# Performance work log

Hardware: AMD Instinct MI355X
Metric: run time of the kernel (lower is better)

The kernel has to match this reference:

```python
import jax, jax.numpy as jnp
import numpy as np
import math

NUM_HEADS = 16
ROPE_BASE = 10000.0


def apply_rope(t):
    # t: [B, H, S, D] with D even. Interleaved-pair rotary embedding (torchtune-style).
    D = t.shape[-1]
    S = t.shape[-2]
    inv_freq = 1.0 / (ROPE_BASE ** (jnp.arange(0, D, 2, dtype=jnp.float32) / D))  # [D/2]
    angles = jnp.arange(S, dtype=jnp.float32)[:, None] * inv_freq[None, :]  # [S, D/2]
    cos = jnp.cos(angles).astype(t.dtype)  # [S, D/2]
    sin = jnp.sin(angles).astype(t.dtype)
    t1 = t[..., 0::2]  # [B, H, S, D/2]
    t2 = t[..., 1::2]
    r1 = t1 * cos - t2 * sin
    r2 = t1 * sin + t2 * cos
    # interleave back
    out = jnp.stack([r1, r2], axis=-1).reshape(t.shape)
    return out


def setup_inputs() -> dict:
    key = jax.random.key(0)
    ks = jax.random.split(key, 6)
    B, S, D = 4, 2048, 2048
    s_in = 1.0 / math.sqrt(D)
    x = jax.random.normal(ks[0], (B, S, D), dtype=jnp.float32)
    wq = jax.random.normal(ks[1], (D, D), dtype=jnp.float32) * s_in
    wk = jax.random.normal(ks[2], (D, D), dtype=jnp.float32) * s_in
    wv = jax.random.normal(ks[3], (D, D), dtype=jnp.float32) * s_in
    wo = jax.random.normal(ks[4], (D, D), dtype=jnp.float32) * s_in
    bo = jnp.zeros((D,), dtype=jnp.float32)
    return {"x": x, "wq": wq, "wk": wk, "wv": wv, "wo": wo, "bo": bo}


def reference(x, wq, wk, wv, wo, bo):
    B, S, D = x.shape
    H = NUM_HEADS
    hd = D // H
    # QKV projections (nn.Linear: y = x @ W^T)
    q = (x @ wq.T).reshape(B, S, H, hd).transpose(0, 2, 1, 3)  # [B,H,S,hd]
    k = (x @ wk.T).reshape(B, S, H, hd).transpose(0, 2, 1, 3)
    v = (x @ wv.T).reshape(B, S, H, hd).transpose(0, 2, 1, 3)
    q = apply_rope(q)
    k = apply_rope(k)
    # causal SDPA (dropout_p = 0 in eval)
    scale = 1.0 / math.sqrt(hd)
    scores = jnp.einsum('bhqd,bhkd->bhqk', q, k) * scale  # [B,H,S,S]
    causal = jnp.tril(jnp.ones((S, S), dtype=bool))
    scores = jnp.where(causal, scores, jnp.finfo(scores.dtype).min)
    attn = jax.nn.softmax(scores, axis=-1)
    ctx = jnp.einsum('bhqk,bhkd->bqhd', attn, v).reshape(B, S, D)
    return ctx @ wo.T + bo
```

## Files before the change

kernel.cpp:

```cpp
#include <hip/hip_runtime.h>

typedef short short8 __attribute__((ext_vector_type(8)));
typedef float f32x4 __attribute__((ext_vector_type(4)));
typedef unsigned int u32x4 __attribute__((ext_vector_type(4)));
typedef unsigned short u16x4 __attribute__((ext_vector_type(4)));
typedef unsigned short u16x8 __attribute__((ext_vector_type(8)));

__device__ __forceinline__ unsigned short f2bf(float f) {
  unsigned int u = __builtin_bit_cast(unsigned int, f);
  u += 0x7fffu + ((u >> 16) & 1u);
  return (unsigned short)(u >> 16);
}
__device__ __forceinline__ float bf2f(unsigned short h) {
  unsigned int u = ((unsigned int)h) << 16;
  return __builtin_bit_cast(float, u);
}

__device__ __forceinline__ void gl16(const unsigned short* g, unsigned short* l) {
  __builtin_amdgcn_global_load_lds((const __attribute__((address_space(1))) unsigned int*)g,
                                   (__attribute__((address_space(3))) unsigned int*)l, 16, 0, 0);
}

#define BB 4
#define SS 2048
#define DD 2048
#define HH 16
#define HD 128
#define MM (BB * SS)

__global__ void cast_all(const float* __restrict__ x, const float* __restrict__ wq,
                         const float* __restrict__ wk, const float* __restrict__ wv,
                         const float* __restrict__ wo, unsigned short* __restrict__ xb,
                         unsigned short* __restrict__ wqb, unsigned short* __restrict__ wkb,
                         unsigned short* __restrict__ wvb, unsigned short* __restrict__ wob) {
  int i = blockIdx.x * blockDim.x + threadIdx.x;
  const int X4 = (MM * DD) / 4;
  const int W4 = (DD * DD) / 4;
  const float* src;
  unsigned short* dst;
  int off;
  if (i < X4) {
    src = x; dst = xb; off = i;
  } else {
    int t = i - X4;
    int w = t >> 20;
    off = t & (W4 - 1);
    src = (w == 0) ? wq : (w == 1) ? wk : (w == 2) ? wv : wo;
    dst = (w == 0) ? wqb : (w == 1) ? wkb : (w == 2) ? wvb : wob;
  }
  f32x4 v = ((const f32x4*)src)[off];
  u16x4 o;
  o[0] = f2bf(v[0]); o[1] = f2bf(v[1]); o[2] = f2bf(v[2]); o[3] = f2bf(v[3]);
  ((u16x4*)dst)[off] = o;
}

#define STGH(P, R0, t, h, moff)                                                     \
  do {                                                                              \
    const unsigned short* _s =                                                      \
        (P) + (size_t)((R0) + (h) * 128 + srow) * DD + (size_t)((t) * 64 + scol);   \
    gl16(_s, lds + (moff) + (h) * 8192 + wvi * 512);                                \
    gl16(_s + (size_t)64 * DD, lds + (moff) + (h) * 8192 + 4096 + wvi * 512);       \
  } while (0)

#define BARRIER asm volatile("s_barrier" ::: "memory")

__device__ __forceinline__ void gemm_core(const unsigned short* __restrict__ Ap,
                                          const unsigned short* __restrict__ Bp,
                                          unsigned short* lds, int rt, int ct,
                                          f32x4 (&acc)[8][4]) {
  const int tid = threadIdx.x;
  const int lane = tid & 63, wvi = tid >> 6;
  const int wm = wvi >> 2, wn = wvi & 3;
  const int quad = lane >> 4, l16 = lane & 15;
  const int srow = wvi * 8 + (lane >> 3);
  const int scol = ((lane & 7) ^ (lane >> 3)) << 3;
  const int ck0 = (quad ^ (l16 & 7)) << 3;
  const int ck1 = ((4 + quad) ^ (l16 & 7)) << 3;
  const int aro = (wm * 128 + l16) << 6;
  const int bro = (wn * 64 + l16) << 6;
  const int rb = rt * 256, cb = ct * 256;

#pragma unroll
  for (int i = 0; i < 8; ++i)
#pragma unroll
    for (int j = 0; j < 4; ++j) acc[i][j] = f32x4{0.f, 0.f, 0.f, 0.f};

  STGH(Bp, cb, 0, 0, 16384);
  STGH(Bp, cb, 0, 1, 16384);
  STGH(Ap, rb, 0, 0, 0);
  STGH(Ap, rb, 0, 1, 0);
  STGH(Bp, cb, 1, 0, 49152);
  STGH(Bp, cb, 1, 1, 49152);
  asm volatile("s_waitcnt vmcnt(4)" ::: "memory");
  BARRIER;

#pragma unroll 2
  for (int t = 0; t < 32; ++t) {
    const unsigned short* ab = lds + ((t & 1) << 15);
    const unsigned short* bb = ab + 16384;
    const int pn = ((t + 1) & 1) << 15;
    const int pc = ((t & 1) << 15) + 16384;
    short8 aq[4][2], b0f[2][2], b1f[2][2];

#pragma unroll
    for (int mi = 0; mi < 4; ++mi) {
      aq[mi][0] = __builtin_bit_cast(short8, *(const u32x4*)(ab + aro + mi * 1024 + ck0));
      aq[mi][1] = __builtin_bit_cast(short8, *(const u32x4*)(ab + aro + mi * 1024 + ck1));
    }
#pragma unroll
    for (int ni = 0; ni < 2; ++ni) {
      b0f[ni][0] = __builtin_bit_cast(short8, *(const u32x4*)(bb + bro + ni * 1024 + ck0));
      b0f[ni][1] = __builtin_bit_cast(short8, *(const u32x4*)(bb + bro + ni * 1024 + ck1));
    }
    if (t < 31) STGH(Ap, rb, t + 1, 0, pn);
    BARRIER;
    __builtin_amdgcn_s_setprio(1);
#pragma unroll
    for (int k = 0; k < 2; ++k)
#pragma unroll
      for (int mi = 0; mi < 4; ++mi)
#pragma unroll
        for (int ni = 0; ni < 2; ++ni)
          acc[mi][ni] =
              __builtin_amdgcn_mfma_f32_16x16x32_bf16(aq[mi][k], b0f[ni][k], acc[mi][ni], 0, 0, 0);
    __builtin_amdgcn_s_setprio(0);
    BARRIER;

#pragma unroll
    for (int ni = 0; ni < 2; ++ni) {
      b1f[ni][0] = __builtin_bit_cast(short8, *(const u32x4*)(bb + bro + 2048 + ni * 1024 + ck0));
      b1f[ni][1] = __builtin_bit_cast(short8, *(const u32x4*)(bb + bro + 2048 + ni * 1024 + ck1));
    }
    if (t < 31) STGH(Ap, rb, t + 1, 1, pn);
    BARRIER;
    __builtin_amdgcn_s_setprio(1);
#pragma unroll
    for (int k = 0; k < 2; ++k)
#pragma unroll
      for (int mi = 0; mi < 4; ++mi)
#pragma unroll
        for (int ni = 0; ni < 2; ++ni)
          acc[mi][2 + ni] = __builtin_amdgcn_mfma_f32_16x16x32_bf16(aq[mi][k], b1f[ni][k],
                                                                    acc[mi][2 + ni], 0, 0, 0);
    __builtin_amdgcn_s_setprio(0);
    BARRIER;

#pragma unroll
    for (int mi = 0; mi < 4; ++mi) {
      aq[mi][0] = __builtin_bit_cast(short8, *(const u32x4*)(ab + aro + 4096 + mi * 1024 + ck0));
      aq[mi][1] = __builtin_bit_cast(short8, *(const u32x4*)(ab + aro + 4096 + mi * 1024 + ck1));
    }
    if (t < 30) STGH(Bp, cb, t + 2, 0, pc);
    BARRIER;
    __builtin_amdgcn_s_setprio(1);
#pragma unroll
    for (int k = 0; k < 2; ++k)
#pragma unroll
      for (int mi = 0; mi < 4; ++mi)
#pragma unroll
        for (int ni = 0; ni < 2; ++ni)
          acc[4 + mi][2 + ni] = __builtin_amdgcn_mfma_f32_16x16x32_bf16(
              aq[mi][k], b1f[ni][k], acc[4 + mi][2 + ni], 0, 0, 0);
    __builtin_amdgcn_s_setprio(0);
    BARRIER;

    if (t < 30) STGH(Bp, cb, t + 2, 1, pc);
    BARRIER;
    __builtin_amdgcn_s_setprio(1);
#pragma unroll
    for (int k = 0; k < 2; ++k)
#pragma unroll
      for (int mi = 0; mi < 4; ++mi)
#pragma unroll
        for (int ni = 0; ni < 2; ++ni)
          acc[4 + mi][ni] = __builtin_amdgcn_mfma_f32_16x16x32_bf16(aq[mi][k], b0f[ni][k],
                                                                    acc[4 + mi][ni], 0, 0, 0);
    __builtin_amdgcn_s_setprio(0);
    if (t < 30) {
      asm volatile("s_waitcnt vmcnt(4)" ::: "memory");
      BARRIER;
    } else if (t == 30) {
      asm volatile("s_waitcnt vmcnt(0)" ::: "memory");
      BARRIER;
    }
  }
}

__global__ __launch_bounds__(512, 2) void gemm_qkv(const unsigned short* __restrict__ A,
                                                   const unsigned short* __restrict__ W0,
                                                   const unsigned short* __restrict__ W1,
                                                   const unsigned short* __restrict__ W2,
                                                   unsigned short* __restrict__ q_out,
                                                   unsigned short* __restrict__ k_out,
                                                   unsigned short* __restrict__ v_out) {
  __shared__ unsigned short lds[65536];
  const int id = (blockIdx.z << 8) | (blockIdx.y << 3) | blockIdx.x;
  const int nid = (id & 7) * 96 + (id >> 3);
  const int z = nid >> 8;
  const int rt = (nid & 255) >> 3, ct = nid & 7;
  const unsigned short* W = (z == 0) ? W0 : (z == 1) ? W1 : W2;
  unsigned short* outb = (z == 0) ? q_out : (z == 1) ? k_out : v_out;
  f32x4 acc[8][4];
  gemm_core(A, W, lds, rt, ct, acc);

  const int tid = threadIdx.x;
  const int lane = tid & 63, wvi = tid >> 6;
  const int wm = wvi >> 2, wn = wvi & 3;
  const int quad = lane >> 4, l16 = lane & 15;

  if (z == 2) {
#pragma unroll
    for (int mi = 0; mi < 8; ++mi)
#pragma unroll
      for (int ni = 0; ni < 4; ++ni)
#pragma unroll
        for (int r = 0; r < 4; ++r) {
          int row_g = rt * 256 + wm * 128 + mi * 16 + quad * 4 + r;
          int col_g = ct * 256 + wn * 64 + ni * 16 + l16;
          int b = row_g >> 11, s = row_g & (SS - 1);
          int h = col_g >> 7, d = col_g & (HD - 1);
          outb[(((size_t)(b * HH + h)) * SS + (size_t)s) * HD + (size_t)d] = f2bf(acc[mi][ni][r]);
        }
  } else {
    const float psc = (z == 0) ? 0.08838834764831845f : 1.0f;
    const bool odd = (l16 & 1) != 0;
    const float nl = -0.14391156831212936f;
    float inv4[4];
#pragma unroll
    for (int ni = 0; ni < 4; ++ni)
      inv4[ni] = __expf((float)((((wn * 64 + ni * 16 + l16) & 127) >> 1)) * nl);
#pragma unroll
    for (int mi = 0; mi < 8; ++mi)
#pragma unroll
      for (int ni = 0; ni < 4; ++ni)
#pragma unroll
        for (int r = 0; r < 4; ++r) {
          int row_g = rt * 256 + wm * 128 + mi * 16 + quad * 4 + r;
          int col_g = ct * 256 + wn * 64 + ni * 16 + l16;
          int b = row_g >> 11, s = row_g & (SS - 1);
          int h = col_g >> 7, d = col_g & (HD - 1);
          float v = acc[mi][ni][r];
          float p = __shfl_xor(v, 1, 64);
          float ang = (float)s * inv4[ni];
          float cs = __cosf(ang), sn = __sinf(ang);
          float o = (odd ? (p * sn + v * cs) : (v * cs - p * sn)) * psc;
          size_t rowbase = (((size_t)(b * HH + h)) * SS + (size_t)s) * HD;
          if (z == 1) {
            outb[rowbase + (size_t)((((d >> 3) ^ (s & 7)) << 3) | (d & 7))] = f2bf(o);
          } else {
            outb[rowbase + (size_t)d] = f2bf(o);
          }
        }
  }
}

__global__ __launch_bounds__(512, 2) void gemm_out(const unsigned short* __restrict__ A,
                                                   const unsigned short* __restrict__ W,
                                                   float* __restrict__ outf,
                                                   const float* __restrict__ bias) {
  __shared__ unsigned short lds[65536];
  const int id = (blockIdx.y << 3) | blockIdx.x;
  const int nid = (id & 7) * 32 + (id >> 3);
  const int rt = nid >> 3, ct = nid & 7;
  f32x4 acc[8][4];
  gemm_core(A, W, lds, rt, ct, acc);

  const int tid = threadIdx.x;
  const int lane = tid & 63, wvi = tid >> 6;
  const int wm = wvi >> 2, wn = wvi & 3;
  const int quad = lane >> 4, l16 = lane & 15;
#pragma unroll
  for (int mi = 0; mi < 8; ++mi)
#pragma unroll
    for (int ni = 0; ni < 4; ++ni)
#pragma unroll
      for (int r = 0; r < 4; ++r) {
        int row_g = rt * 256 + wm * 128 + mi * 16 + quad * 4 + r;
        int col_g = ct * 256 + wn * 64 + ni * 16 + l16;
        outf[(size_t)row_g * DD + col_g] = acc[mi][ni][r] + bias[col_g];
      }
}

__global__ __launch_bounds__(512, 2) void attn_kernel(const unsigned short* __restrict__ qb,
                                                      const unsigned short* __restrict__ kb,
                                                      const unsigned short* __restrict__ vb,
                                                      unsigned short* __restrict__ ctxb) {
  __shared__ unsigned short lds[40960];
  const int tid = threadIdx.x;
  const int g0 = blockIdx.x;
  const int g = (g0 & 7) * 128 + (g0 >> 3);
  const int bh = g >> 4;
  const int qa = 15 - (g & 15);
  const int lane = tid & 63, wvi = tid >> 6;
  const int quad = lane >> 4, l16 = lane & 15;
  const size_t bhq = (size_t)bh * SS * HD;
  const int qrow = qa * 128 + wvi * 16;
  const int b = bh >> 4, h = bh & (HH - 1);
  unsigned short* Pw = lds + 32768 + wvi * 1024;
  const int vrr = tid & 31, vcd = tid >> 5;
  const int krow = wvi * 4 + (lane >> 4);
  const int kcol = (lane & 15) * 8;
  f32x4 zero = {0.f, 0.f, 0.f, 0.f};

  short8 qf[4];
#pragma unroll
  for (int ks = 0; ks < 4; ++ks)
    qf[ks] = __builtin_bit_cast(
        short8, *(const u32x4*)(qb + bhq + (size_t)(qrow + l16) * HD + ks * 32 + quad * 8));

  f32x4 acc[8];
#pragma unroll
  for (int dt = 0; dt < 8; ++dt) acc[dt] = zero;
  float lpart[4] = {0.f, 0.f, 0.f, 0.f};

  const int ntile = 2 * qa + 2;

  {
    const unsigned short* vsrc = vb + bhq + (size_t)(2 * vrr) * HD + vcd * 8;
    u32x4 pva = *(const u32x4*)vsrc;
    u32x4 pvb = *(const u32x4*)(vsrc + HD);
    gl16(kb + bhq + (size_t)krow * HD + kcol, lds + krow * 128);
    gl16(kb + bhq + (size_t)(32 + krow) * HD + kcol, lds + (32 + krow) * 128);
    u16x8 va = __builtin_bit_cast(u16x8, pva);
    u16x8 vb2 = __builtin_bit_cast(u16x8, pvb);
    unsigned int* vw = (unsigned int*)(lds + 16384);
#pragma unroll
    for (int j = 0; j < 8; ++j)
      vw[(vcd * 8 + j) * 32 + (((vrr >> 2) ^ j) << 2) + (vrr & 3)] =
          (unsigned int)va[j] | ((unsigned int)vb2[j] << 16);
    __syncthreads();
  }

  for (int kt = 0; kt < ntile; ++kt) {
    const int kv0 = kt * 64;
    const int cur = (kt & 1) * 8192;
    const int nxt = ((kt + 1) & 1) * 8192;
    const unsigned short* Kc = lds + cur;
    const unsigned short* Vc = lds + 16384 + cur;
    const bool hasnext = (kt + 1 < ntile);

    u32x4 pva, pvb;
    if (hasnext) {
      const int kvn = kv0 + 64;
      const unsigned short* vsrc = vb + bhq + (size_t)(kvn + 2 * vrr) * HD + vcd * 8;
      pva = *(const u32x4*)vsrc;
      pvb = *(const u32x4*)(vsrc + HD);
      gl16(kb + bhq + (size_t)(kvn + krow) * HD + kcol, lds + nxt + krow * 128);
      gl16(kb + bhq + (size_t)(kvn + 32 + krow) * HD + kcol, lds + nxt + (32 + krow) * 128);
    }

    f32x4 sc[4];
#pragma unroll
    for (int nt = 0; nt < 4; ++nt) {
      sc[nt] = zero;
#pragma unroll
      for (int ks = 0; ks < 4; ++ks) {
        short8 kf = __builtin_bit_cast(
            short8, *(const u32x4*)(Kc + (nt * 16 + l16) * 128 +
                                    (((ks * 4 + quad) ^ (l16 & 7)) << 3)));
        sc[nt] = __builtin_amdgcn_mfma_f32_16x16x32_bf16(qf[ks], kf, sc[nt], 0, 0, 0);
      }
    }

    const bool dm = (kt >= ntile - 2);
    if (dm) {
#pragma unroll
      for (int r = 0; r < 4; ++r) {
        int row = qrow + quad * 4 + r;
        int prow = quad * 4 + r;
#pragma unroll
        for (int nt = 0; nt < 4; ++nt) {
          int col = kv0 + nt * 16 + l16;
          float pv = (col > row) ? 0.f : __expf(sc[nt][r]);
          lpart[r] += pv;
          int el = prow * 64 +
                   ((((nt * 2 + (l16 >> 3)) + prow + 4 * (prow >> 3)) & 7) << 3) + (l16 & 7);
          Pw[el] = f2bf(pv);
        }
      }
    } else {
#pragma unroll
      for (int r = 0; r < 4; ++r) {
        int prow = quad * 4 + r;
#pragma unroll
        for (int nt = 0; nt < 4; ++nt) {
          float pv = __expf(sc[nt][r]);
          lpart[r] += pv;
          int el = prow * 64 +
                   ((((nt * 2 + (l16 >> 3)) + prow + 4 * (prow >> 3)) & 7) << 3) + (l16 & 7);
          Pw[el] = f2bf(pv);
        }
      }
    }

#pragma unroll
    for (int ks2 = 0; ks2 < 2; ++ks2) {
      short8 pfrag = __builtin_bit_cast(
          short8, *(const u32x4*)(Pw + l16 * 64 +
                                  ((((ks2 * 4 + quad) + l16 + 4 * (l16 >> 3)) & 7) << 3)));
#pragma unroll
      for (int dt = 0; dt < 8; ++dt) {
        short8 vf = __builtin_bit_cast(
            short8, *(const u32x4*)(Vc + (dt * 16 + l16) * 64 +
                                    (((ks2 * 4 + quad) ^ (l16 & 7)) << 3)));
        acc[dt] = __builtin_amdgcn_mfma_f32_16x16x32_bf16(pfrag, vf, acc[dt], 0, 0, 0);
      }
    }

    if (hasnext) {
      u16x8 va = __builtin_bit_cast(u16x8, pva);
      u16x8 vb2 = __builtin_bit_cast(u16x8, pvb);
      unsigned int* vw = (unsigned int*)(lds + 16384 + nxt);
#pragma unroll
      for (int j = 0; j < 8; ++j)
        vw[(vcd * 8 + j) * 32 + (((vrr >> 2) ^ j) << 2) + (vrr & 3)] =
            (unsigned int)va[j] | ((unsigned int)vb2[j] << 16);
    }
    __syncthreads();
  }

  float rl[4];
#pragma unroll
  for (int r = 0; r < 4; ++r) {
    float rs = lpart[r];
#pragma unroll
    for (int off = 1; off < 16; off <<= 1) rs += __shfl_xor(rs, off, 64);
    rl[r] = 1.0f / rs;
  }
#pragma unroll
  for (int dt = 0; dt < 8; ++dt)
#pragma unroll
    for (int r = 0; r < 4; ++r) {
      int row = qrow + quad * 4 + r;
      ctxb[((size_t)(b * SS + row)) * DD + h * HD + dt * 16 + l16] = f2bf(acc[dt][r] * rl[r]);
    }
}

extern "C" void kernel_launch(void* const* d_in, const int* in_sizes, int n_in,
                              void* d_out, int out_size, void* d_ws, size_t ws_size,
                              hipStream_t stream) {
  const float* x = (const float*)d_in[0];
  const float* wq = (const float*)d_in[1];
  const float* wk = (const float*)d_in[2];
  const float* wv = (const float*)d_in[3];
  const float* wo = (const float*)d_in[4];
  const float* bo = (const float*)d_in[5];
  float* out = (float*)d_out;

  unsigned short* xb = (unsigned short*)d_ws;
  unsigned short* wqb = xb + (size_t)MM * DD;
  unsigned short* wkb = wqb + (size_t)DD * DD;
  unsigned short* wvb = wkb + (size_t)DD * DD;
  unsigned short* wob = wvb + (size_t)DD * DD;
  unsigned short* qb = wob + (size_t)DD * DD;
  unsigned short* kb = qb + (size_t)MM * DD;
  unsigned short* vb = kb + (size_t)MM * DD;
  unsigned short* ctxb = vb + (size_t)MM * DD;

  cast_all<<<(2 * MM * DD / 4) / 256, 256, 0, stream>>>(x, wq, wk, wv, wo, xb, wqb, wkb, wvb, wob);

  dim3 gg(DD / 256, MM / 256, 3);
  gemm_qkv<<<gg, 512, 0, stream>>>(xb, wqb, wkb, wvb, qb, kb, vb);

  attn_kernel<<<1024, 512, 0, stream>>>(qb, kb, vb, ctxb);

  dim3 go(DD / 256, MM / 256);
  gemm_out<<<go, 512, 0, stream>>>(ctxb, wob, out, bo);
}
```

Measured before the change: 559.2 us.

## Give each attention wave two 16-row query blocks with 256-thread blocks

Attention blocks shrink from 8 waves to 4, and each wave now handles 32 query rows as two 16-row blocks. Every K and V fragment read from LDS is reused across two MFMAs, which halves LDS fragment traffic per unit of compute. V is no longer double-buffered: a single V tile is overwritten after an extra barrier, which frees LDS but serialises the V store behind the PV compute. Register pressure roughly doubles for the accumulators and score tiles.

```diff
diff --git a/kernel.cpp b/kernel.cpp
--- a/kernel.cpp
+++ b/kernel.cpp
@@ -281,11 +281,11 @@
       }
 }
 
-__global__ __launch_bounds__(512, 2) void attn_kernel(const unsigned short* __restrict__ qb,
+__global__ __launch_bounds__(256, 2) void attn_kernel(const unsigned short* __restrict__ qb,
                                                       const unsigned short* __restrict__ kb,
                                                       const unsigned short* __restrict__ vb,
                                                       unsigned short* __restrict__ ctxb) {
-  __shared__ unsigned short lds[40960];
+  __shared__ unsigned short lds[32768];
   const int tid = threadIdx.x;
   const int g0 = blockIdx.x;
   const int g = (g0 & 7) * 128 + (g0 >> 3);
@@ -294,71 +294,101 @@
   const int lane = tid & 63, wvi = tid >> 6;
   const int quad = lane >> 4, l16 = lane & 15;
   const size_t bhq = (size_t)bh * SS * HD;
-  const int qrow = qa * 128 + wvi * 16;
+  const int qrow = qa * 128 + wvi * 32;
   const int b = bh >> 4, h = bh & (HH - 1);
-  unsigned short* Pw = lds + 32768 + wvi * 1024;
-  const int vrr = tid & 31, vcd = tid >> 5;
-  const int krow = wvi * 4 + (lane >> 4);
-  const int kcol = (lane & 15) * 8;
+  unsigned short* Pw = lds + 24576 + wvi * 2048;
+  unsigned short* Vt = lds + 16384;
+  const int kcol = l16 * 8;
   f32x4 zero = {0.f, 0.f, 0.f, 0.f};
 
-  short8 qf[4];
-#pragma unroll
-  for (int ks = 0; ks < 4; ++ks)
-    qf[ks] = __builtin_bit_cast(
-        short8, *(const u32x4*)(qb + bhq + (size_t)(qrow + l16) * HD + ks * 32 + quad * 8));
-
-  f32x4 acc[8];
-#pragma unroll
-  for (int dt = 0; dt < 8; ++dt) acc[dt] = zero;
-  float lpart[4] = {0.f, 0.f, 0.f, 0.f};
+  short8 qf[2][4];
+#pragma unroll
+  for (int rb = 0; rb < 2; ++rb)
+#pragma unroll
+    for (int ks = 0; ks < 4; ++ks)
+      qf[rb][ks] = __builtin_bit_cast(
+          short8,
+          *(const u32x4*)(qb + bhq + (size_t)(qrow + rb * 16 + l16) * HD + ks * 32 + quad * 8));
+
+  f32x4 acc[2][8];
+#pragma unroll
+  for (int rb = 0; rb < 2; ++rb)
+#pragma unroll
+    for (int dt = 0; dt < 8; ++dt) acc[rb][dt] = zero;
+  float lpart[2][4] = {{0.f, 0.f, 0.f, 0.f}, {0.f, 0.f, 0.f, 0.f}};
 
   const int ntile = 2 * qa + 2;
 
   {
-    const unsigned short* vsrc = vb + bhq + (size_t)(2 * vrr) * HD + vcd * 8;
-    u32x4 pva = *(const u32x4*)vsrc;
-    u32x4 pvb = *(const u32x4*)(vsrc + HD);
-    gl16(kb + bhq + (size_t)krow * HD + kcol, lds + krow * 128);
-    gl16(kb + bhq + (size_t)(32 + krow) * HD + kcol, lds + (32 + krow) * 128);
-    u16x8 va = __builtin_bit_cast(u16x8, pva);
-    u16x8 vb2 = __builtin_bit_cast(u16x8, pvb);
-    unsigned int* vw = (unsigned int*)(lds + 16384);
-#pragma unroll
-    for (int j = 0; j < 8; ++j)
-      vw[(vcd * 8 + j) * 32 + (((vrr >> 2) ^ j) << 2) + (vrr & 3)] =
-          (unsigned int)va[j] | ((unsigned int)vb2[j] << 16);
+    u32x4 pva0, pvb0, pva1, pvb1;
+    {
+      const unsigned short* vs0 = vb + bhq + (size_t)(2 * (tid & 31)) * HD + (tid >> 5) * 8;
+      pva0 = *(const u32x4*)vs0;
+      pvb0 = *(const u32x4*)(vs0 + HD);
+      const int u = tid + 256;
+      const unsigned short* vs1 = vb + bhq + (size_t)(2 * (u & 31)) * HD + (u >> 5) * 8;
+      pva1 = *(const u32x4*)vs1;
+      pvb1 = *(const u32x4*)(vs1 + HD);
+    }
+#pragma unroll
+    for (int r = 0; r < 4; ++r)
+      gl16(kb + bhq + (size_t)(r * 16 + wvi * 4 + quad) * HD + kcol,
+           lds + (r * 16 + wvi * 4) * 128);
+    unsigned int* vw = (unsigned int*)Vt;
+    {
+      int rr = tid & 31, c = tid >> 5;
+      u16x8 va = __builtin_bit_cast(u16x8, pva0);
+      u16x8 vb2 = __builtin_bit_cast(u16x8, pvb0);
+#pragma unroll
+      for (int j = 0; j < 8; ++j)
+        vw[(c * 8 + j) * 32 + (((rr >> 2) ^ j) << 2) + (rr & 3)] =
+            (unsigned int)va[j] | ((unsigned int)vb2[j] << 16);
+      const int u = tid + 256;
+      rr = u & 31; c = u >> 5;
+      va = __builtin_bit_cast(u16x8, pva1);
+      vb2 = __builtin_bit_cast(u16x8, pvb1);
+#pragma unroll
+      for (int j = 0; j < 8; ++j)
+        vw[(c * 8 + j) * 32 + (((rr >> 2) ^ j) << 2) + (rr & 3)] =
+            (unsigned int)va[j] | ((unsigned int)vb2[j] << 16);
+    }
     __syncthreads();
   }
 
   for (int kt = 0; kt < ntile; ++kt) {
     const int kv0 = kt * 64;
-    const int cur = (kt & 1) * 8192;
+    const unsigned short* Kc = lds + (kt & 1) * 8192;
     const int nxt = ((kt + 1) & 1) * 8192;
-    const unsigned short* Kc = lds + cur;
-    const unsigned short* Vc = lds + 16384 + cur;
     const bool hasnext = (kt + 1 < ntile);
 
-    u32x4 pva, pvb;
+    u32x4 pva0, pvb0, pva1, pvb1;
     if (hasnext) {
       const int kvn = kv0 + 64;
-      const unsigned short* vsrc = vb + bhq + (size_t)(kvn + 2 * vrr) * HD + vcd * 8;
-      pva = *(const u32x4*)vsrc;
-      pvb = *(const u32x4*)(vsrc + HD);
-      gl16(kb + bhq + (size_t)(kvn + krow) * HD + kcol, lds + nxt + krow * 128);
-      gl16(kb + bhq + (size_t)(kvn + 32 + krow) * HD + kcol, lds + nxt + (32 + krow) * 128);
-    }
-
-    f32x4 sc[4];
+      const unsigned short* vs0 = vb + bhq + (size_t)(kvn + 2 * (tid & 31)) * HD + (tid >> 5) * 8;
+      pva0 = *(const u32x4*)vs0;
+      pvb0 = *(const u32x4*)(vs0 + HD);
+      const int u = tid + 256;
+      const unsigned short* vs1 = vb + bhq + (size_t)(kvn + 2 * (u & 31)) * HD + (u >> 5) * 8;
+      pva1 = *(const u32x4*)vs1;
+      pvb1 = *(const u32x4*)(vs1 + HD);
+#pragma unroll
+      for (int r = 0; r < 4; ++r)
+        gl16(kb + bhq + (size_t)(kvn + r * 16 + wvi * 4 + quad) * HD + kcol,
+             lds + nxt + (r * 16 + wvi * 4) * 128);
+    }
+
+    f32x4 sc0[4], sc1[4];
 #pragma unroll
     for (int nt = 0; nt < 4; ++nt) {
-      sc[nt] = zero;
+      sc0[nt] = zero;
+      sc1[nt] = zero;
 #pragma unroll
       for (int ks = 0; ks < 4; ++ks) {
         short8 kf = __builtin_bit_cast(
             short8, *(const u32x4*)(Kc + (nt * 16 + l16) * 128 +
                                     (((ks * 4 + quad) ^ (l16 & 7)) << 3)));
-        sc[nt] = __builtin_amdgcn_mfma_f32_16x16x32_bf16(qf[ks], kf, sc[nt], 0, 0, 0);
+        sc0[nt] = __builtin_amdgcn_mfma_f32_16x16x32_bf16(qf[0][ks], kf, sc0[nt], 0, 0, 0);
+        sc1[nt] = __builtin_amdgcn_mfma_f32_16x16x32_bf16(qf[1][ks], kf, sc1[nt], 0, 0, 0);
       }
     }
 
@@ -366,74 +396,95 @@
     if (dm) {
 #pragma unroll
       for (int r = 0; r < 4; ++r) {
-        int row = qrow + quad * 4 + r;
-        int prow = quad * 4 + r;
+        int p15 = quad * 4 + r;
 #pragma unroll
         for (int nt = 0; nt < 4; ++nt) {
           int col = kv0 + nt * 16 + l16;
-          float pv = (col > row) ? 0.f : __expf(sc[nt][r]);
-          lpart[r] += pv;
-          int el = prow * 64 +
-                   ((((nt * 2 + (l16 >> 3)) + prow + 4 * (prow >> 3)) & 7) << 3) + (l16 & 7);
-          Pw[el] = f2bf(pv);
+          int el = p15 * 64 + ((((nt * 2 + (l16 >> 3)) + p15 + 4 * (p15 >> 3)) & 7) << 3) +
+                   (l16 & 7);
+          float pv0 = (col > qrow + p15) ? 0.f : __expf(sc0[nt][r]);
+          lpart[0][r] += pv0;
+          Pw[el] = f2bf(pv0);
+          float pv1 = (col > qrow + 16 + p15) ? 0.f : __expf(sc1[nt][r]);
+          lpart[1][r] += pv1;
+          Pw[1024 + el] = f2bf(pv1);
         }
       }
     } else {
 #pragma unroll
       for (int r = 0; r < 4; ++r) {
-        int prow = quad * 4 + r;
+        int p15 = quad * 4 + r;
 #pragma unroll
         for (int nt = 0; nt < 4; ++nt) {
-          float pv = __expf(sc[nt][r]);
-          lpart[r] += pv;
-          int el = prow * 64 +
-                   ((((nt * 2 + (l16 >> 3)) + prow + 4 * (prow >> 3)) & 7) << 3) + (l16 & 7);
-          Pw[el] = f2bf(pv);
+          int el = p15 * 64 + ((((nt * 2 + (l16 >> 3)) + p15 + 4 * (p15 >> 3)) & 7) << 3) +
+                   (l16 & 7);
+          float pv0 = __expf(sc0[nt][r]);
+          lpart[0][r] += pv0;
+          Pw[el] = f2bf(pv0);
+          float pv1 = __expf(sc1[nt][r]);
+          lpart[1][r] += pv1;
+          Pw[1024 + el] = f2bf(pv1);
         }
       }
     }
 
 #pragma unroll
     for (int ks2 = 0; ks2 < 2; ++ks2) {
-      short8 pfrag = __builtin_bit_cast(
-          short8, *(const u32x4*)(Pw + l16 * 64 +
-                                  ((((ks2 * 4 + quad) + l16 + 4 * (l16 >> 3)) & 7) << 3)));
+      const int pk = (((ks2 * 4 + quad) + l16 + 4 * (l16 >> 3)) & 7) << 3;
+      short8 pf0 = __builtin_bit_cast(short8, *(const u32x4*)(Pw + l16 * 64 + pk));
+      short8 pf1 = __builtin_bit_cast(short8, *(const u32x4*)(Pw + 1024 + l16 * 64 + pk));
 #pragma unroll
       for (int dt = 0; dt < 8; ++dt) {
         short8 vf = __builtin_bit_cast(
-            short8, *(const u32x4*)(Vc + (dt * 16 + l16) * 64 +
+            short8, *(const u32x4*)(Vt + (dt * 16 + l16) * 64 +
                                     (((ks2 * 4 + quad) ^ (l16 & 7)) << 3)));
-        acc[dt] = __builtin_amdgcn_mfma_f32_16x16x32_bf16(pfrag, vf, acc[dt], 0, 0, 0);
+        acc[0][dt] = __builtin_amdgcn_mfma_f32_16x16x32_bf16(pf0, vf, acc[0][dt], 0, 0, 0);
+        acc[1][dt] = __builtin_amdgcn_mfma_f32_16x16x32_bf16(pf1, vf, acc[1][dt], 0, 0, 0);
       }
     }
 
+    __syncthreads();
+
     if (hasnext) {
-      u16x8 va = __builtin_bit_cast(u16x8, pva);
-      u16x8 vb2 = __builtin_bit_cast(u16x8, pvb);
-      unsigned int* vw = (unsigned int*)(lds + 16384 + nxt);
+      unsigned int* vw = (unsigned int*)Vt;
+      int rr = tid & 31, c = tid >> 5;
+      u16x8 va = __builtin_bit_cast(u16x8, pva0);
+      u16x8 vb2 = __builtin_bit_cast(u16x8, pvb0);
 #pragma unroll
       for (int j = 0; j < 8; ++j)
-        vw[(vcd * 8 + j) * 32 + (((vrr >> 2) ^ j) << 2) + (vrr & 3)] =
+        vw[(c * 8 + j) * 32 + (((rr >> 2) ^ j) << 2) + (rr & 3)] =
             (unsigned int)va[j] | ((unsigned int)vb2[j] << 16);
-    }
-    __syncthreads();
+      const int u = tid + 256;
+      rr = u & 31; c = u >> 5;
+      va = __builtin_bit_cast(u16x8, pva1);
+      vb2 = __builtin_bit_cast(u16x8, pvb1);
+#pragma unroll
+      for (int j = 0; j < 8; ++j)
+        vw[(c * 8 + j) * 32 + (((rr >> 2) ^ j) << 2) + (rr & 3)] =
+            (unsigned int)va[j] | ((unsigned int)vb2[j] << 16);
+      __syncthreads();
+    }
   }
 
-  float rl[4];
-#pragma unroll
-  for (int r = 0; r < 4; ++r) {
-    float rs = lpart[r];
-#pragma unroll
-    for (int off = 1; off < 16; off <<= 1) rs += __shfl_xor(rs, off, 64);
-    rl[r] = 1.0f / rs;
+#pragma unroll
+  for (int rb = 0; rb < 2; ++rb) {
+    float rl[4];
+#pragma unroll
+    for (int r = 0; r < 4; ++r) {
+      float rs = lpart[rb][r];
+#pragma unroll
+      for (int off = 1; off < 16; off <<= 1) rs += __shfl_xor(rs, off, 64);
+      rl[r] = 1.0f / rs;
+    }
+#pragma unroll
+    for (int dt = 0; dt < 8; ++dt)
+#pragma unroll
+      for (int r = 0; r < 4; ++r) {
+        int row = qrow + rb * 16 + quad * 4 + r;
+        ctxb[((size_t)(b * SS + row)) * DD + h * HD + dt * 16 + l16] =
+            f2bf(acc[rb][dt][r] * rl[r]);
+      }
   }
-#pragma unroll
-  for (int dt = 0; dt < 8; ++dt)
-#pragma unroll
-    for (int r = 0; r < 4; ++r) {
-      int row = qrow + quad * 4 + r;
-      ctxb[((size_t)(b * SS + row)) * DD + h * HD + dt * 16 + l16] = f2bf(acc[dt][r] * rl[r]);
-    }
 }
 
 extern "C" void kernel_launch(void* const* d_in, const int* in_sizes, int n_in,
@@ -462,7 +513,7 @@
   dim3 gg(DD / 256, MM / 256, 3);
   gemm_qkv<<<gg, 512, 0, stream>>>(xb, wqb, wkb, wvb, qb, kb, vb);
 
-  attn_kernel<<<1024, 512, 0, stream>>>(qb, kb, vb, ctxb);
+  attn_kernel<<<1024, 256, 0, stream>>>(qb, kb, vb, ctxb);
 
   dim3 go(DD / 256, MM / 256);
   gemm_out<<<go, 512, 0, stream>>>(ctxb, wob, out, bo);
```

Result: faster. 542.0 us (-3.1%).
